# Optimization experiments

Hardware: AMD Instinct MI355X
Metric: run time of the kernel (lower is better)

## Reference

```python
import jax, jax.numpy as jnp
import numpy as np

N_DENSE = 13
N_SPARSE = 26
VOCAB = 100000
EMB_DIM = 64
ATTN_HIDDEN = 12
BATCH = 8192
TEMP = 0.1

# pair indices (i < j) over the 26 sparse fields -> 325 pairs
_ROW, _COL = np.triu_indices(N_SPARSE, k=1)


def setup_inputs() -> dict:
    key = jax.random.key(0)
    ks = jax.random.split(key, 10)
    return {
        "dense_x": jax.random.normal(ks[0], (BATCH, N_DENSE), dtype=jnp.float32),
        "sparse_idx": jax.random.randint(ks[1], (BATCH, N_SPARSE), 0, VOCAB, dtype=jnp.int32),
        "emb_tables": jax.random.normal(ks[2], (N_SPARSE, VOCAB, EMB_DIM), dtype=jnp.float32) * 0.01,
        "attn_W": jax.random.normal(ks[3], (EMB_DIM, ATTN_HIDDEN), dtype=jnp.float32) * 0.1,
        "attn_b": jnp.zeros((ATTN_HIDDEN,), dtype=jnp.float32),
        "proj_W": jax.random.normal(ks[4], (ATTN_HIDDEN, 1), dtype=jnp.float32) * 0.1,
        "proj_b": jnp.zeros((1,), dtype=jnp.float32),
        "lin_W": jax.random.normal(ks[5], (N_DENSE + N_SPARSE, 1), dtype=jnp.float32) * 0.01,
        "lin_b": jnp.zeros((1,), dtype=jnp.float32),
        "pred_W": jax.random.normal(ks[6], (EMB_DIM, 1), dtype=jnp.float32) * 0.1,
        "pred_b": jnp.zeros((1,), dtype=jnp.float32),
    }


def reference(dense_x, sparse_idx, emb_tables, attn_W, attn_b, proj_W, proj_b,
              lin_W, lin_b, pred_W, pred_b):
    # linear part operates on the raw concatenated input (sparse ids as floats,
    # exactly as the torch module does via linear_part(x))
    x = jnp.concatenate([dense_x, sparse_idx.astype(jnp.float32)], axis=1)  # [B, 39]
    part_1 = x @ lin_W + lin_b  # [B, 1]

    # per-field embedding gather: [B, 26, D]
    field_ids = jnp.arange(N_SPARSE)[None, :]
    emb = emb_tables[field_ids, sparse_idx]

    # pairwise element-wise cross products: [B, 325, D]
    cross = emb[:, _ROW, :] * emb[:, _COL, :]

    # attention MLP + softmax over pairs (temperature 0.1)
    h = jax.nn.relu(cross @ attn_W + attn_b)            # [B, 325, 12]
    logits = (h @ proj_W + proj_b) / TEMP               # [B, 325, 1]
    scores = jax.nn.softmax(logits, axis=1)

    att_out = jnp.sum(cross * scores, axis=1)           # [B, D]
    part_2 = att_out @ pred_W + pred_b                  # [B, 1]
    return jax.nn.sigmoid(part_1 + part_2)
```

## Files before the change

### kernel.cpp

```cpp
#include <hip/hip_runtime.h>
#include <math.h>

#define N_DENSE  13
#define N_SPARSE 26
#define VOCAB    100000
#define EMB      64
#define NH       12
#define NPAIR    325
#define NTILE    21
#define NPADH    336
#define EBROW    72
#define EBSLOT   1888
#define TEMP_INV 10.0f

typedef __attribute__((ext_vector_type(8))) _Float16 f16x8;
typedef __attribute__((ext_vector_type(4))) float    f32x4;

__device__ __forceinline__ int ebbase(int f) { return f * EBROW + (((f >> 3) & 3) << 3); }

__global__ __launch_bounds__(128, 4) void afm_kernel(
    const float* __restrict__ dense_x,
    const int*   __restrict__ sparse_idx,
    const float* __restrict__ emb,
    const float* __restrict__ attn_W,
    const float* __restrict__ attn_b,
    const float* __restrict__ proj_W,
    const float* __restrict__ proj_b,
    const float* __restrict__ lin_W,
    const float* __restrict__ lin_b,
    const float* __restrict__ pred_W,
    const float* __restrict__ pred_b,
    float* __restrict__ out)
{
    const int tid  = threadIdx.x;
    const int lane = tid & 63;
    const int wv   = tid >> 6;
    const int q    = lane >> 4;
    const int c16  = lane & 15;
    const int row0 = __builtin_amdgcn_readfirstlane(blockIdx.x * 4 + wv * 2);

    __shared__ __align__(16) unsigned short eb_s[2][2][EBSLOT];
    __shared__ __align__(16) unsigned short ptab_s[NPADH];

    unsigned short* ebw0 = &eb_s[wv][0][0];
    unsigned short* ebw1 = &eb_s[wv][1][0];

    int l32 = lane & 31;
    int myid = (l32 < N_SPARSE)
             ? sparse_idx[(row0 + (lane >> 5)) * N_SPARSE + l32] : 0;

    float4 vg[13];
    #pragma unroll
    for (int k = 0; k < 13; ++k) {
        int q2   = lane + 64 * k;
        int rsel = q2 >= 416;
        int loc  = q2 - (rsel ? 416 : 0);
        int f = loc >> 4, d4 = loc & 15;
        int idk = __shfl(myid, (rsel << 5) + f);
        vg[k] = *(reinterpret_cast<const float4*>(
                    emb + ((size_t)f * VOCAB + (size_t)idk) * EMB) + d4);
    }

    f16x8 wf[2];
    {
        #pragma unroll
        for (int kt = 0; kt < 2; ++kt) {
            union { f16x8 v; unsigned u32[4]; } u;
            #pragma unroll
            for (int jp = 0; jp < 4; ++jp) {
                int d0 = kt * 32 + q * 8 + jp * 2;
                float w0, w1;
                if (c16 < NH)       { w0 = attn_W[d0 * NH + c16];
                                      w1 = attn_W[(d0 + 1) * NH + c16]; }
                else if (c16 == NH) { w0 = pred_W[d0];
                                      w1 = pred_W[d0 + 1]; }
                else                { w0 = 0.f; w1 = 0.f; }
                auto hh = __builtin_amdgcn_cvt_pkrtz(w0, w1);
                __builtin_memcpy(&u.u32[jp], &hh, 4);
            }
            wf[kt] = u.v;
        }
    }
    float b4[4], pwh[4];
    #pragma unroll
    for (int r = 0; r < 4; ++r) {
        int h = q * 4 + r;
        bool ok = (h < NH);
        b4[r]  = ok ? attn_b[h] : 0.0f;
        pwh[r] = ok ? proj_W[h] : 0.0f;
    }
    const float pb = proj_b[0];

    #pragma unroll 1
    for (int p = lane; p < NPADH; p += 64) {
        int pc = p < NPAIR ? p : NPAIR - 1;
        float sf = sqrtf((float)(2601 - 8 * pc));
        int i = (int)((51.0f - sf) * 0.5f);
        int st = (i * (51 - i)) >> 1;
        if (pc < st) { --i; st = (i * (51 - i)) >> 1; }
        else { int st2 = ((i + 1) * (50 - i)) >> 1; if (pc >= st2) { ++i; st = st2; } }
        int j = i + 1 + (pc - st);
        ptab_s[p] = (unsigned short)(i | (j << 8));
    }

    int srcf  = lane - N_DENSE;
    bool idok = (srcf >= 0 && srcf < N_SPARSE);
    int id0 = __shfl(myid, idok ? srcf : 0);
    int id1 = __shfl(myid, 32 + (idok ? srcf : 0));
    float p1t0 = 0.0f, p1t1 = 0.0f;
    if (lane < N_DENSE) {
        p1t0 = dense_x[row0 * N_DENSE + lane] * lin_W[lane];
        p1t1 = dense_x[(row0 + 1) * N_DENSE + lane] * lin_W[lane];
    } else if (lane < N_DENSE + N_SPARSE) {
        p1t0 = (float)id0 * lin_W[lane];
        p1t1 = (float)id1 * lin_W[lane];
    }

    #pragma unroll
    for (int k = 0; k < 13; ++k) {
        int q2   = lane + 64 * k;
        int rsel = q2 >= 416;
        int loc  = q2 - (rsel ? 416 : 0);
        int f = loc >> 4, d4 = loc & 15;
        auto h01 = __builtin_amdgcn_cvt_pkrtz(vg[k].x, vg[k].y);
        auto h23 = __builtin_amdgcn_cvt_pkrtz(vg[k].z, vg[k].w);
        uint2 pk;
        __builtin_memcpy(&pk.x, &h01, 4);
        __builtin_memcpy(&pk.y, &h23, 4);
        unsigned short* dst = rsel ? ebw1 : ebw0;
        *reinterpret_cast<uint2*>(&dst[ebbase(f) + d4 * 4]) = pk;
    }

    float lsum0 = 0.0f, vsum0 = 0.0f, lsum1 = 0.0f, vsum1 = 0.0f;
    #pragma unroll 2
    for (int t = 0; t < NTILE; ++t) {
        unsigned pt = ptab_s[t * 16 + c16];
        int i = pt & 0xff, j = pt >> 8;
        const int bi = ebbase(i), bj = ebbase(j);
        const bool pv = (t * 16 + c16) < NPAIR;

        const f16x8* pi0 = reinterpret_cast<const f16x8*>(ebw0 + bi);
        const f16x8* pj0 = reinterpret_cast<const f16x8*>(ebw0 + bj);
        const f16x8* pi1 = reinterpret_cast<const f16x8*>(ebw1 + bi);
        const f16x8* pj1 = reinterpret_cast<const f16x8*>(ebw1 + bj);
        f16x8 ca0 = pi0[q] * pj0[q], cb0 = pi0[q + 4] * pj0[q + 4];
        f16x8 ca1 = pi1[q] * pj1[q], cb1 = pi1[q + 4] * pj1[q + 4];

        __builtin_amdgcn_s_setprio(1);
        f32x4 acc0 = {0.f, 0.f, 0.f, 0.f};
        f32x4 acc1 = {0.f, 0.f, 0.f, 0.f};
        acc0 = __builtin_amdgcn_mfma_f32_16x16x32_f16(wf[0], ca0, acc0, 0, 0, 0);
        acc1 = __builtin_amdgcn_mfma_f32_16x16x32_f16(wf[0], ca1, acc1, 0, 0, 0);
        acc0 = __builtin_amdgcn_mfma_f32_16x16x32_f16(wf[1], cb0, acc0, 0, 0, 0);
        acc1 = __builtin_amdgcn_mfma_f32_16x16x32_f16(wf[1], cb1, acc1, 0, 0, 0);
        __builtin_amdgcn_s_setprio(0);

        float par0 =       fmaxf(acc0[0] + b4[0], 0.f) * pwh[0];
        par0 = fmaf(fmaxf(acc0[1] + b4[1], 0.f), pwh[1], par0);
        par0 = fmaf(fmaxf(acc0[2] + b4[2], 0.f), pwh[2], par0);
        par0 = fmaf(fmaxf(acc0[3] + b4[3], 0.f), pwh[3], par0);
        float par1 =       fmaxf(acc1[0] + b4[0], 0.f) * pwh[0];
        par1 = fmaf(fmaxf(acc1[1] + b4[1], 0.f), pwh[1], par1);
        par1 = fmaf(fmaxf(acc1[2] + b4[2], 0.f), pwh[2], par1);
        par1 = fmaf(fmaxf(acc1[3] + b4[3], 0.f), pwh[3], par1);

        par0 += __shfl_xor(par0, 16);
        par1 += __shfl_xor(par1, 16);
        par0 += __shfl_xor(par0, 32);
        par1 += __shfl_xor(par1, 32);

        float ev0 = __expf((par0 + pb) * TEMP_INV);
        float ev1 = __expf((par1 + pb) * TEMP_INV);
        ev0 = pv ? ev0 : 0.0f;
        ev1 = pv ? ev1 : 0.0f;
        lsum0 += ev0;
        lsum1 += ev1;
        float m0 = (q == 3) ? acc0[0] : 0.0f;
        float m1 = (q == 3) ? acc1[0] : 0.0f;
        vsum0 = fmaf(ev0, m0, vsum0);
        vsum1 = fmaf(ev1, m1, vsum1);
    }

    #pragma unroll
    for (int o = 32; o > 0; o >>= 1) {
        lsum0 += __shfl_xor(lsum0, o);
        vsum0 += __shfl_xor(vsum0, o);
        lsum1 += __shfl_xor(lsum1, o);
        vsum1 += __shfl_xor(vsum1, o);
        p1t0  += __shfl_xor(p1t0, o);
        p1t1  += __shfl_xor(p1t1, o);
    }
    if (lane == 0) {
        float z0 = p1t0 + lin_b[0] + 4.0f * vsum0 / lsum0 + pred_b[0];
        float z1 = p1t1 + lin_b[0] + 4.0f * vsum1 / lsum1 + pred_b[0];
        out[row0]     = 1.0f / (1.0f + __expf(-z0));
        out[row0 + 1] = 1.0f / (1.0f + __expf(-z1));
    }
}

extern "C" void kernel_launch(void* const* d_in, const int* in_sizes, int n_in,
                              void* d_out, int out_size, void* d_ws, size_t ws_size,
                              hipStream_t stream)
{
    const float* dense_x = (const float*)d_in[0];
    const int*   sparse  = (const int*)  d_in[1];
    const float* emb     = (const float*)d_in[2];
    const float* attn_W  = (const float*)d_in[3];
    const float* attn_b  = (const float*)d_in[4];
    const float* proj_W  = (const float*)d_in[5];
    const float* proj_b  = (const float*)d_in[6];
    const float* lin_W   = (const float*)d_in[7];
    const float* lin_b   = (const float*)d_in[8];
    const float* pred_W  = (const float*)d_in[9];
    const float* pred_b  = (const float*)d_in[10];
    float* out = (float*)d_out;

    int rows = in_sizes[0] / N_DENSE;
    afm_kernel<<<rows / 4, 128, 0, stream>>>(dense_x, sparse, emb, attn_W, attn_b,
                                             proj_W, proj_b, lin_W, lin_b,
                                             pred_W, pred_b, out);
}
```

Measured before the change: 30.17 us.

## Process four rows per wave, prefetching second pair's embeddings during first compute

Each wave now handles four rows as two row pairs. The gather for the second pair is issued into registers before the tile loop runs on the first pair, so global-memory latency overlaps with MFMA compute. Grid size is halved and launch bounds drop to 2 blocks per SM to make room for the extra 13 float4 registers. Fewer resident waves may reduce latency hiding elsewhere, and the shared-buffer reuse depends on the wave's own ordering since there is no barrier.

```diff
diff --git a/kernel.cpp b/kernel.cpp
--- a/kernel.cpp
+++ b/kernel.cpp
@@ -18,7 +18,65 @@
 
 __device__ __forceinline__ int ebbase(int f) { return f * EBROW + (((f >> 3) & 3) << 3); }
 
-__global__ __launch_bounds__(128, 4) void afm_kernel(
+__device__ __forceinline__ void tile_loop(
+    const unsigned short* __restrict__ ebw0,
+    const unsigned short* __restrict__ ebw1,
+    const unsigned short* __restrict__ ptab,
+    const f16x8& wf0, const f16x8& wf1,
+    const float* b4, const float* pwh, float pb, int q, int c16,
+    float& lsum0, float& vsum0, float& lsum1, float& vsum1)
+{
+    #pragma unroll 2
+    for (int t = 0; t < NTILE; ++t) {
+        unsigned pt = ptab[t * 16 + c16];
+        int i = pt & 0xff, j = pt >> 8;
+        const int bi = ebbase(i), bj = ebbase(j);
+        const bool pv = (t * 16 + c16) < NPAIR;
+
+        const f16x8* pi0 = reinterpret_cast<const f16x8*>(ebw0 + bi);
+        const f16x8* pj0 = reinterpret_cast<const f16x8*>(ebw0 + bj);
+        const f16x8* pi1 = reinterpret_cast<const f16x8*>(ebw1 + bi);
+        const f16x8* pj1 = reinterpret_cast<const f16x8*>(ebw1 + bj);
+        f16x8 ca0 = pi0[q] * pj0[q], cb0 = pi0[q + 4] * pj0[q + 4];
+        f16x8 ca1 = pi1[q] * pj1[q], cb1 = pi1[q + 4] * pj1[q + 4];
+
+        __builtin_amdgcn_s_setprio(1);
+        f32x4 acc0 = {0.f, 0.f, 0.f, 0.f};
+        f32x4 acc1 = {0.f, 0.f, 0.f, 0.f};
+        acc0 = __builtin_amdgcn_mfma_f32_16x16x32_f16(wf0, ca0, acc0, 0, 0, 0);
+        acc1 = __builtin_amdgcn_mfma_f32_16x16x32_f16(wf0, ca1, acc1, 0, 0, 0);
+        acc0 = __builtin_amdgcn_mfma_f32_16x16x32_f16(wf1, cb0, acc0, 0, 0, 0);
+        acc1 = __builtin_amdgcn_mfma_f32_16x16x32_f16(wf1, cb1, acc1, 0, 0, 0);
+        __builtin_amdgcn_s_setprio(0);
+
+        float par0 =       fmaxf(acc0[0] + b4[0], 0.f) * pwh[0];
+        par0 = fmaf(fmaxf(acc0[1] + b4[1], 0.f), pwh[1], par0);
+        par0 = fmaf(fmaxf(acc0[2] + b4[2], 0.f), pwh[2], par0);
+        par0 = fmaf(fmaxf(acc0[3] + b4[3], 0.f), pwh[3], par0);
+        float par1 =       fmaxf(acc1[0] + b4[0], 0.f) * pwh[0];
+        par1 = fmaf(fmaxf(acc1[1] + b4[1], 0.f), pwh[1], par1);
+        par1 = fmaf(fmaxf(acc1[2] + b4[2], 0.f), pwh[2], par1);
+        par1 = fmaf(fmaxf(acc1[3] + b4[3], 0.f), pwh[3], par1);
+
+        par0 += __shfl_xor(par0, 16);
+        par1 += __shfl_xor(par1, 16);
+        par0 += __shfl_xor(par0, 32);
+        par1 += __shfl_xor(par1, 32);
+
+        float ev0 = __expf((par0 + pb) * TEMP_INV);
+        float ev1 = __expf((par1 + pb) * TEMP_INV);
+        ev0 = pv ? ev0 : 0.0f;
+        ev1 = pv ? ev1 : 0.0f;
+        lsum0 += ev0;
+        lsum1 += ev1;
+        float m0 = (q == 3) ? acc0[0] : 0.0f;
+        float m1 = (q == 3) ? acc1[0] : 0.0f;
+        vsum0 = fmaf(ev0, m0, vsum0);
+        vsum1 = fmaf(ev1, m1, vsum1);
+    }
+}
+
+__global__ __launch_bounds__(128, 2) void afm_kernel(
     const float* __restrict__ dense_x,
     const int*   __restrict__ sparse_idx,
     const float* __restrict__ emb,
@@ -37,7 +95,7 @@
     const int wv   = tid >> 6;
     const int q    = lane >> 4;
     const int c16  = lane & 15;
-    const int row0 = __builtin_amdgcn_readfirstlane(blockIdx.x * 4 + wv * 2);
+    const int row0 = __builtin_amdgcn_readfirstlane(blockIdx.x * 8 + wv * 4);
 
     __shared__ __align__(16) unsigned short eb_s[2][2][EBSLOT];
     __shared__ __align__(16) unsigned short ptab_s[NPADH];
@@ -45,23 +103,25 @@
     unsigned short* ebw0 = &eb_s[wv][0][0];
     unsigned short* ebw1 = &eb_s[wv][1][0];
 
-    int l32 = lane & 31;
-    int myid = (l32 < N_SPARSE)
-             ? sparse_idx[(row0 + (lane >> 5)) * N_SPARSE + l32] : 0;
+    int l32  = lane & 31;
+    int rsel = lane >> 5;
+    bool idv = (l32 < N_SPARSE);
+    int idA = idv ? sparse_idx[(row0 + rsel) * N_SPARSE + l32] : 0;
+    int idB = idv ? sparse_idx[(row0 + 2 + rsel) * N_SPARSE + l32] : 0;
 
     float4 vg[13];
     #pragma unroll
     for (int k = 0; k < 13; ++k) {
         int q2   = lane + 64 * k;
-        int rsel = q2 >= 416;
-        int loc  = q2 - (rsel ? 416 : 0);
-        int f = loc >> 4, d4 = loc & 15;
-        int idk = __shfl(myid, (rsel << 5) + f);
+        int rs   = q2 >= 416;
+        int loc  = q2 - (rs ? 416 : 0);
+        int f = loc >> 4, d4 = loc & 15;
+        int idk = __shfl(idA, (rs << 5) + f);
         vg[k] = *(reinterpret_cast<const float4*>(
                     emb + ((size_t)f * VOCAB + (size_t)idk) * EMB) + d4);
     }
 
-    f16x8 wf[2];
+    f16x8 wf0, wf1;
     {
         #pragma unroll
         for (int kt = 0; kt < 2; ++kt) {
@@ -78,7 +138,7 @@
                 auto hh = __builtin_amdgcn_cvt_pkrtz(w0, w1);
                 __builtin_memcpy(&u.u32[jp], &hh, 4);
             }
-            wf[kt] = u.v;
+            if (kt == 0) wf0 = u.v; else wf1 = u.v;
         }
     }
     float b4[4], pwh[4];
@@ -105,96 +165,106 @@
 
     int srcf  = lane - N_DENSE;
     bool idok = (srcf >= 0 && srcf < N_SPARSE);
-    int id0 = __shfl(myid, idok ? srcf : 0);
-    int id1 = __shfl(myid, 32 + (idok ? srcf : 0));
-    float p1t0 = 0.0f, p1t1 = 0.0f;
+    int sidx0 = idok ? srcf : 0;
+    int s0A = __shfl(idA, sidx0);
+    int s1A = __shfl(idA, 32 + sidx0);
+    int s0B = __shfl(idB, sidx0);
+    int s1B = __shfl(idB, 32 + sidx0);
+    float p1t[4] = {0.f, 0.f, 0.f, 0.f};
     if (lane < N_DENSE) {
-        p1t0 = dense_x[row0 * N_DENSE + lane] * lin_W[lane];
-        p1t1 = dense_x[(row0 + 1) * N_DENSE + lane] * lin_W[lane];
+        #pragma unroll
+        for (int r = 0; r < 4; ++r)
+            p1t[r] = dense_x[(row0 + r) * N_DENSE + lane] * lin_W[lane];
     } else if (lane < N_DENSE + N_SPARSE) {
-        p1t0 = (float)id0 * lin_W[lane];
-        p1t1 = (float)id1 * lin_W[lane];
-    }
-
-    #pragma unroll
-    for (int k = 0; k < 13; ++k) {
-        int q2   = lane + 64 * k;
-        int rsel = q2 >= 416;
-        int loc  = q2 - (rsel ? 416 : 0);
+        float lw = lin_W[lane];
+        p1t[0] = (float)s0A * lw;
+        p1t[1] = (float)s1A * lw;
+        p1t[2] = (float)s0B * lw;
+        p1t[3] = (float)s1B * lw;
+    }
+
+    #pragma unroll
+    for (int k = 0; k < 13; ++k) {
+        int q2   = lane + 64 * k;
+        int rs   = q2 >= 416;
+        int loc  = q2 - (rs ? 416 : 0);
         int f = loc >> 4, d4 = loc & 15;
         auto h01 = __builtin_amdgcn_cvt_pkrtz(vg[k].x, vg[k].y);
         auto h23 = __builtin_amdgcn_cvt_pkrtz(vg[k].z, vg[k].w);
         uint2 pk;
         __builtin_memcpy(&pk.x, &h01, 4);
         __builtin_memcpy(&pk.y, &h23, 4);
-        unsigned short* dst = rsel ? ebw1 : ebw0;
+        unsigned short* dst = rs ? ebw1 : ebw0;
         *reinterpret_cast<uint2*>(&dst[ebbase(f) + d4 * 4]) = pk;
     }
 
-    float lsum0 = 0.0f, vsum0 = 0.0f, lsum1 = 0.0f, vsum1 = 0.0f;
-    #pragma unroll 2
-    for (int t = 0; t < NTILE; ++t) {
-        unsigned pt = ptab_s[t * 16 + c16];
-        int i = pt & 0xff, j = pt >> 8;
-        const int bi = ebbase(i), bj = ebbase(j);
-        const bool pv = (t * 16 + c16) < NPAIR;
-
-        const f16x8* pi0 = reinterpret_cast<const f16x8*>(ebw0 + bi);
-        const f16x8* pj0 = reinterpret_cast<const f16x8*>(ebw0 + bj);
-        const f16x8* pi1 = reinterpret_cast<const f16x8*>(ebw1 + bi);
-        const f16x8* pj1 = reinterpret_cast<const f16x8*>(ebw1 + bj);
-        f16x8 ca0 = pi0[q] * pj0[q], cb0 = pi0[q + 4] * pj0[q + 4];
-        f16x8 ca1 = pi1[q] * pj1[q], cb1 = pi1[q + 4] * pj1[q + 4];
-
-        __builtin_amdgcn_s_setprio(1);
-        f32x4 acc0 = {0.f, 0.f, 0.f, 0.f};
-        f32x4 acc1 = {0.f, 0.f, 0.f, 0.f};
-        acc0 = __builtin_amdgcn_mfma_f32_16x16x32_f16(wf[0], ca0, acc0, 0, 0, 0);
-        acc1 = __builtin_amdgcn_mfma_f32_16x16x32_f16(wf[0], ca1, acc1, 0, 0, 0);
-        acc0 = __builtin_amdgcn_mfma_f32_16x16x32_f16(wf[1], cb0, acc0, 0, 0, 0);
-        acc1 = __builtin_amdgcn_mfma_f32_16x16x32_f16(wf[1], cb1, acc1, 0, 0, 0);
-        __builtin_amdgcn_s_setprio(0);
-
-        float par0 =       fmaxf(acc0[0] + b4[0], 0.f) * pwh[0];
-        par0 = fmaf(fmaxf(acc0[1] + b4[1], 0.f), pwh[1], par0);
-        par0 = fmaf(fmaxf(acc0[2] + b4[2], 0.f), pwh[2], par0);
-        par0 = fmaf(fmaxf(acc0[3] + b4[3], 0.f), pwh[3], par0);
-        float par1 =       fmaxf(acc1[0] + b4[0], 0.f) * pwh[0];
-        par1 = fmaf(fmaxf(acc1[1] + b4[1], 0.f), pwh[1], par1);
-        par1 = fmaf(fmaxf(acc1[2] + b4[2], 0.f), pwh[2], par1);
-        par1 = fmaf(fmaxf(acc1[3] + b4[3], 0.f), pwh[3], par1);
-
-        par0 += __shfl_xor(par0, 16);
-        par1 += __shfl_xor(par1, 16);
-        par0 += __shfl_xor(par0, 32);
-        par1 += __shfl_xor(par1, 32);
-
-        float ev0 = __expf((par0 + pb) * TEMP_INV);
-        float ev1 = __expf((par1 + pb) * TEMP_INV);
-        ev0 = pv ? ev0 : 0.0f;
-        ev1 = pv ? ev1 : 0.0f;
-        lsum0 += ev0;
-        lsum1 += ev1;
-        float m0 = (q == 3) ? acc0[0] : 0.0f;
-        float m1 = (q == 3) ? acc1[0] : 0.0f;
-        vsum0 = fmaf(ev0, m0, vsum0);
-        vsum1 = fmaf(ev1, m1, vsum1);
-    }
-
-    #pragma unroll
-    for (int o = 32; o > 0; o >>= 1) {
-        lsum0 += __shfl_xor(lsum0, o);
-        vsum0 += __shfl_xor(vsum0, o);
-        lsum1 += __shfl_xor(lsum1, o);
-        vsum1 += __shfl_xor(vsum1, o);
-        p1t0  += __shfl_xor(p1t0, o);
-        p1t1  += __shfl_xor(p1t1, o);
-    }
-    if (lane == 0) {
-        float z0 = p1t0 + lin_b[0] + 4.0f * vsum0 / lsum0 + pred_b[0];
-        float z1 = p1t1 + lin_b[0] + 4.0f * vsum1 / lsum1 + pred_b[0];
-        out[row0]     = 1.0f / (1.0f + __expf(-z0));
-        out[row0 + 1] = 1.0f / (1.0f + __expf(-z1));
+    float4 vh[13];
+    #pragma unroll
+    for (int k = 0; k < 13; ++k) {
+        int q2   = lane + 64 * k;
+        int rs   = q2 >= 416;
+        int loc  = q2 - (rs ? 416 : 0);
+        int f = loc >> 4, d4 = loc & 15;
+        int idk = __shfl(idB, (rs << 5) + f);
+        vh[k] = *(reinterpret_cast<const float4*>(
+                    emb + ((size_t)f * VOCAB + (size_t)idk) * EMB) + d4);
+    }
+
+    float lsA0 = 0.f, vsA0 = 0.f, lsA1 = 0.f, vsA1 = 0.f;
+    tile_loop(ebw0, ebw1, ptab_s, wf0, wf1, b4, pwh, pb, q, c16,
+              lsA0, vsA0, lsA1, vsA1);
+
+    asm volatile("" ::: "memory");
+
+    #pragma unroll
+    for (int k = 0; k < 13; ++k) {
+        int q2   = lane + 64 * k;
+        int rs   = q2 >= 416;
+        int loc  = q2 - (rs ? 416 : 0);
+        int f = loc >> 4, d4 = loc & 15;
+        auto h01 = __builtin_amdgcn_cvt_pkrtz(vh[k].x, vh[k].y);
+        auto h23 = __builtin_amdgcn_cvt_pkrtz(vh[k].z, vh[k].w);
+        uint2 pk;
+        __builtin_memcpy(&pk.x, &h01, 4);
+        __builtin_memcpy(&pk.y, &h23, 4);
+        unsigned short* dst = rs ? ebw1 : ebw0;
+        *reinterpret_cast<uint2*>(&dst[ebbase(f) + d4 * 4]) = pk;
+    }
+
+    {
+        float a = lsA0, b = vsA0, c = lsA1, d = vsA1, e = p1t[0], f2 = p1t[1];
+        #pragma unroll
+        for (int o = 32; o > 0; o >>= 1) {
+            a += __shfl_xor(a, o); b += __shfl_xor(b, o);
+            c += __shfl_xor(c, o); d += __shfl_xor(d, o);
+            e += __shfl_xor(e, o); f2 += __shfl_xor(f2, o);
+        }
+        if (lane == 0) {
+            float z0 = e + lin_b[0] + 4.0f * b / a + pred_b[0];
+            float z1 = f2 + lin_b[0] + 4.0f * d / c + pred_b[0];
+            out[row0]     = 1.0f / (1.0f + __expf(-z0));
+            out[row0 + 1] = 1.0f / (1.0f + __expf(-z1));
+        }
+    }
+
+    float lsB0 = 0.f, vsB0 = 0.f, lsB1 = 0.f, vsB1 = 0.f;
+    tile_loop(ebw0, ebw1, ptab_s, wf0, wf1, b4, pwh, pb, q, c16,
+              lsB0, vsB0, lsB1, vsB1);
+
+    {
+        float a = lsB0, b = vsB0, c = lsB1, d = vsB1, e = p1t[2], f2 = p1t[3];
+        #pragma unroll
+        for (int o = 32; o > 0; o >>= 1) {
+            a += __shfl_xor(a, o); b += __shfl_xor(b, o);
+            c += __shfl_xor(c, o); d += __shfl_xor(d, o);
+            e += __shfl_xor(e, o); f2 += __shfl_xor(f2, o);
+        }
+        if (lane == 0) {
+            float z2 = e + lin_b[0] + 4.0f * b / a + pred_b[0];
+            float z3 = f2 + lin_b[0] + 4.0f * d / c + pred_b[0];
+            out[row0 + 2] = 1.0f / (1.0f + __expf(-z2));
+            out[row0 + 3] = 1.0f / (1.0f + __expf(-z3));
+        }
     }
 }
 
@@ -216,7 +286,7 @@
     float* out = (float*)d_out;
 
     int rows = in_sizes[0] / N_DENSE;
-    afm_kernel<<<rows / 4, 128, 0, stream>>>(dense_x, sparse, emb, attn_W, attn_b,
+    afm_kernel<<<rows / 8, 128, 0, stream>>>(dense_x, sparse, emb, attn_W, attn_b,
                                              proj_W, proj_b, lin_W, lin_b,
                                              pred_W, pred_b, out);
 }
```

Result: slower. 32.20 us (+6.7%).
